# Performance work log

Measured on AMD Instinct MI355X. Metric: run time of the kernel, lower is better.

The kernel has to match this reference:

```python
import jax, jax.numpy as jnp
import numpy as np
from jax import lax

TAU_MIN = 0.01
TAU_MAX = 10.0
SLOW_TAU = 5.0


def setup_inputs() -> dict:
    key = jax.random.key(0)
    ks = iter(jax.random.split(key, 40))
    def p(shape, scale=0.05):
        return (jax.random.normal(next(ks), shape, jnp.float32) * scale)
    B, T, D = 1024, 512, 31
    FU, SU, H = 32, 32, 64
    inp = {
        "x": jax.random.normal(next(ks), (B, T, D), jnp.float32),
        # FlashFloodGate: Linear(62->32), Linear(32->1)
        "fg_w1": p((32, 2 * D)), "fg_b1": p((32,)),
        "fg_w2": p((1, 32)), "fg_b2": p((1,)),
        # fast LTC cell
        "fwin": p((FU, D)), "fbin": p((FU,)), "fwrec": p((FU, FU)),
        # slow LTC cell
        "swin": p((SU, D)), "sbin": p((SU,)), "swrec": p((SU, SU)),
        # fusion Linear(64->64)
        "fu_w": p((H, FU + SU)), "fu_b": p((H,)),
        # attention Linear(64->32), Linear(32->1)
        "at_w1": p((32, H)), "at_b1": p((32,)),
        "at_w2": p((1, 32)), "at_b2": p((1,)),
        # depth head Linear(64->64), Linear(64->5)
        "d_w1": p((64, H)), "d_b1": p((64,)),
        "d_w2": p((5, 64)), "d_b2": p((5,)),
        # overflow head Linear(64->64), Linear(64->32), Linear(32->1)
        "o_w1": p((64, H)), "o_b1": p((64,)),
        "o_w2": p((32, 64)), "o_b2": p((32,)),
        "o_w3": p((1, 32)), "o_b3": p((1,)),
        # intensity head Linear(64->32), Linear(32->1)
        "i_w1": p((32, H)), "i_b1": p((32,)),
        "i_w2": p((1, 32)), "i_b2": p((1,)),
    }
    return inp


def _ltc_scan(pre_tbh, w_rec, tau_tb1, h0):
    # pre_tbh: [T,B,H] precomputed W_in x + b; tau_tb1 broadcastable to [T,B,1]
    def step(h, inp):
        pre_t, tau_t = inp
        upd = jnp.tanh(pre_t + h @ w_rec.T)
        h = h + (upd - h) / tau_t
        return h, h
    _, hs = lax.scan(step, h0, (pre_tbh, tau_tb1))
    return jnp.transpose(hs, (1, 0, 2))  # [B,T,H]


def _forward(x, fg_w1, fg_b1, fg_w2, fg_b2, fwin, fbin, fwrec, swin, sbin, swrec,
             fu_w, fu_b, at_w1, at_b1, at_w2, at_b2, d_w1, d_b1, d_w2, d_b2,
             o_w1, o_b1, o_w2, o_b2, o_w3, o_b3, i_w1, i_b1, i_w2, i_b2):
    B, T, D = x.shape
    # FlashFloodGate over all timesteps (x_prev of t=0 is x_0 -> dx=0)
    dx = jnp.concatenate([jnp.zeros_like(x[:, :1]), x[:, 1:] - x[:, :-1]], axis=1)
    ci = jnp.concatenate([x, dx], axis=-1)                       # [B,T,2D]
    cs = jax.nn.sigmoid(jnp.tanh(ci @ fg_w1.T + fg_b1) @ fg_w2.T + fg_b2)  # [B,T,1]
    tau_fast = TAU_MAX - cs * (TAU_MAX - TAU_MIN)                # [B,T,1]
    # fast LTC (stepwise tau)
    pre_f = jnp.transpose(x @ fwin.T + fbin, (1, 0, 2))          # [T,B,FU]
    fast = _ltc_scan(pre_f, fwrec, jnp.transpose(tau_fast, (1, 0, 2)),
                     jnp.zeros((B, fwrec.shape[0]), x.dtype))
    # slow LTC (constant tau = 5.0, shape [B,1])
    pre_s = jnp.transpose(x @ swin.T + sbin, (1, 0, 2))          # [T,B,SU]
    slow = _ltc_scan(pre_s, swrec, jnp.full((T, 1, 1), SLOW_TAU, x.dtype),
                     jnp.zeros((B, swrec.shape[0]), x.dtype))
    # fusion
    ltc = jnp.tanh(jnp.concatenate([fast, slow], axis=-1) @ fu_w.T + fu_b)  # [B,T,H]
    # attention over time
    logits = jnp.tanh(ltc @ at_w1.T + at_b1) @ at_w2.T + at_b2   # [B,T,1]
    attn = jax.nn.softmax(logits, axis=1)
    context = jnp.sum(ltc * attn, axis=1)                        # [B,H]
    # heads (dropout is identity in eval)
    depths = jax.nn.relu(context @ d_w1.T + d_b1) @ d_w2.T + d_b2
    overflow = jax.nn.sigmoid(
        jax.nn.relu(jax.nn.relu(context @ o_w1.T + o_b1) @ o_w2.T + o_b2) @ o_w3.T + o_b3)
    intensity = jax.nn.sigmoid(jax.nn.relu(context @ i_w1.T + i_b1) @ i_w2.T + i_b2)
    return (depths, overflow, intensity)


def reference(x, fg_w1, fg_b1, fg_w2, fg_b2, fwin, fbin, fwrec, swin, sbin, swrec,
              fu_w, fu_b, at_w1, at_b1, at_w2, at_b2, d_w1, d_b1, d_w2, d_b2,
              o_w1, o_b1, o_w2, o_b2, o_w3, o_b3, i_w1, i_b1, i_w2, i_b2):
    return _forward(x, fg_w1, fg_b1, fg_w2, fg_b2, fwin, fbin, fwrec, swin, sbin,
                    swrec, fu_w, fu_b, at_w1, at_b1, at_w2, at_b2, d_w1, d_b1,
                    d_w2, d_b2, o_w1, o_b1, o_w2, o_b2, o_w3, o_b3,
                    i_w1, i_b1, i_w2, i_b2)
```

## Files before the change

kernel.cpp:

```cpp
#include <hip/hip_runtime.h>


#define T_  512
#define D_  31
#define GR_ 16
#define NG_ 32
#define NIT 35
#define L2E 1.4426950408889634f
#define TS_ 2.8853900817779268f

typedef decltype(__builtin_amdgcn_cvt_pkrtz(0.0f, 0.0f)) h2;
typedef _Float16 h8v __attribute__((ext_vector_type(8)));
typedef float    f4v __attribute__((ext_vector_type(4)));

__device__ __forceinline__ float fexp2(float x){ return __builtin_amdgcn_exp2f(x); }
__device__ __forceinline__ float frcp (float x){ return __builtin_amdgcn_rcpf(x); }
__device__ __forceinline__ float tanh_pre(float x){
    return 1.0f - 2.0f * frcp(1.0f + fexp2(x));
}
__device__ __forceinline__ h2 cvt2(float a, float b){ return __builtin_amdgcn_cvt_pkrtz(a, b); }
__device__ __forceinline__ h2 bch2(unsigned v){ return __builtin_bit_cast(h2, v); }
__device__ __forceinline__ unsigned bcu(h2 v){ return __builtin_bit_cast(unsigned, v); }

template <int CTRL>
__device__ __forceinline__ float dppf(float v){
    int r = __builtin_amdgcn_update_dpp(0, __builtin_bit_cast(int, v),
                                        CTRL, 0xf, 0xf, true);
    return __builtin_bit_cast(float, r);
}
template <int CTRL>
__device__ __forceinline__ unsigned dppu(unsigned v){
    return (unsigned)__builtin_amdgcn_update_dpp(0, (int)v, CTRL, 0xf, 0xf, true);
}
__device__ __forceinline__ unsigned swz16(unsigned v){
    return (unsigned)__builtin_amdgcn_ds_swizzle((int)v, 0x401F);
}
__device__ __forceinline__ float rsum16(float v){
    v += dppf<0xB1>(v); v += dppf<0x4E>(v); v += dppf<0x141>(v); v += dppf<0x140>(v);
    return v;
}

#if __has_builtin(__builtin_amdgcn_fdot2)
#define FDOT2(acc, a, b) (acc) = __builtin_amdgcn_fdot2((a), (b), (acc), false)
#else
#define FDOT2(acc, a, b) (acc) += (float)(a)[0]*(float)(b)[0] + (float)(a)[1]*(float)(b)[1]
#endif

#define MFMA16(A, Bf, Cf) __builtin_amdgcn_mfma_f32_16x16x32_f16((A), (Bf), (Cf), 0, 0, 0)

#define BAR() do { asm volatile("s_waitcnt lgkmcnt(0)" ::: "memory"); \
                   __builtin_amdgcn_s_barrier();                      \
                   asm volatile("" ::: "memory"); } while (0)

__launch_bounds__(256, 4)
__global__ void lnn_mf(
    const float* __restrict__ X,
    const float* __restrict__ fg_w1, const float* __restrict__ fg_b1,
    const float* __restrict__ fg_w2, const float* __restrict__ fg_b2,
    const float* __restrict__ fwin,  const float* __restrict__ fbin,
    const float* __restrict__ fwrec,
    const float* __restrict__ swin,  const float* __restrict__ sbin,
    const float* __restrict__ swrec,
    const float* __restrict__ fu_w,  const float* __restrict__ fu_b,
    const float* __restrict__ at_w1, const float* __restrict__ at_b1,
    const float* __restrict__ at_w2, const float* __restrict__ at_b2,
    const float* __restrict__ d_w1,  const float* __restrict__ d_b1,
    const float* __restrict__ d_w2,  const float* __restrict__ d_b2,
    const float* __restrict__ o_w1,  const float* __restrict__ o_b1,
    const float* __restrict__ o_w2,  const float* __restrict__ o_b2,
    const float* __restrict__ o_w3,  const float* __restrict__ o_b3,
    const float* __restrict__ i_w1,  const float* __restrict__ i_b1,
    const float* __restrict__ i_w2,  const float* __restrict__ i_b2,
    float* __restrict__ out, int B)
{
    const int b    = blockIdx.x;
    const int tx   = threadIdx.x;
    const int wid  = tx >> 6;
    const int lane = tx & 63;
    const int u    = lane & 31;
    const int hb32 = lane & 32;
    const int role = (wid + b) & 3;

    __shared__ __align__(16) float    xr_sh [4][GR_][36];
    __shared__ float    xdm   [36];
    __shared__ __align__(16) float    pre_t [2][64][20];
    __shared__ __align__(16) float    rt4   [2][GR_];
    __shared__ __align__(16) unsigned hpk_sh[2][GR_][36];
    __shared__ __align__(16) unsigned ltcpk [2][GR_][36];
    __shared__ __align__(16) float    pw_sh [GR_];
    __shared__ float    ctx_sh[64];

    if (tx < 64) xr_sh[tx >> 4][tx & 15][31] = 0.0f;

    if (role == 0) {
        const int col = lane & 15, kb = lane >> 4;
        h8v wB[8];
        #pragma unroll
        for (int c = 0; c < 8; ++c) {
            float wv[8];
            #pragma unroll
            for (int j = 0; j < 8; ++j) {
                const int k = kb*8 + j;
                float v = 0.0f;
                if (k < 31) {
                    const int uu = 16*(c & 1) + col;
                    if (c < 2)      v = fg_w1[uu*62 + k] + fg_w1[uu*62 + 31 + k];
                    else if (c < 4) v = fg_w1[uu*62 + 31 + k];
                    else if (c < 6) v = fwin[uu*31 + k];
                    else            v = swin[uu*31 + k];
                }
                wv[j] = v * TS_;
            }
            uint4 qq = { bcu(cvt2(wv[0],wv[1])), bcu(cvt2(wv[2],wv[3])),
                         bcu(cvt2(wv[4],wv[5])), bcu(cvt2(wv[6],wv[7])) };
            wB[c] = __builtin_bit_cast(h8v, qq);
        }
        const float b1c[2] = { fg_b1[col] * TS_, fg_b1[16 + col] * TS_ };
        const float pb[4]  = { fbin[col] * TS_, fbin[16+col] * TS_,
                               sbin[col] * TS_, sbin[16+col] * TS_ };
        const float w2n[2] = { fg_w2[col] * (-L2E), fg_w2[16+col] * (-L2E) };
        const float b2n    = fg_b2[0] * (-L2E);
        const unsigned* Xu = (const unsigned*)(X + (size_t)b * T_ * D_ + lane);
        float ypv[2] = {0.0f, 0.0f};
        asm volatile("s_waitcnt vmcnt(0)" ::: "memory");

        #pragma unroll
        for (int gg = 0; gg < 2; ++gg)
            #pragma unroll
            for (int k = 0; k < GR_; ++k)
                if (lane < 31)
                    __builtin_amdgcn_global_load_lds(
                        (const __attribute__((address_space(1))) unsigned*)(Xu + (size_t)(GR_*gg + k) * 31),
                        (__attribute__((address_space(3))) unsigned*)(&xr_sh[gg][k][0]),
                        4, 0, 0);

        for (int i = 0; i < NIT; ++i) {
            asm volatile("s_waitcnt vmcnt(16)" ::: "memory");
            BAR();
            {
                const int gq = i + 2;
                #pragma unroll
                for (int k = 0; k < GR_; ++k) {
                    int tl = GR_*gq + k; if (tl > 511) tl = 511;
                    float* dst = (gq <= NG_-1) ? &xr_sh[gq & 3][k][0] : &xdm[0];
                    if (lane < 31)
                        __builtin_amdgcn_global_load_lds(
                            (const __attribute__((address_space(1))) unsigned*)(Xu + (size_t)tl * 31),
                            (__attribute__((address_space(3))) unsigned*)dst,
                            4, 0, 0);
                }
            }
            if (i <= NG_-1) {
                const int sG = i & 3;
                const int sP = i & 1;
                const float* xrow = &xr_sh[sG][col][kb*8];
                float4 xa = *(const float4*)xrow;
                float4 xb = *(const float4*)(xrow + 4);
                uint4 aq = { bcu(cvt2(xa.x,xa.y)), bcu(cvt2(xa.z,xa.w)),
                             bcu(cvt2(xb.x,xb.y)), bcu(cvt2(xb.z,xb.w)) };
                h8v Af = __builtin_bit_cast(h8v, aq);
                f4v C[8];
                #pragma unroll
                for (int c = 0; c < 8; ++c) {
                    f4v z = {0.f, 0.f, 0.f, 0.f};
                    C[c] = MFMA16(Af, wB[c], z);
                }
                const int tb = kb * 4;
                float tp[4] = {0.f, 0.f, 0.f, 0.f};
                #pragma unroll
                for (int p = 0; p < 2; ++p) {
                    f4v G = C[p], Y = C[2+p];
                    if (i == 0) ypv[p] = __shfl(Y[0], col);
                    float ylast = __shfl(Y[3], 48 + col);
                    float yup   = __shfl(Y[3], (lane - 16) & 63);
                    float ysh0  = (kb == 0) ? ypv[p] : yup;
                    float h1v[4];
                    h1v[0] = tanh_pre(G[0] - ysh0 + b1c[p]);
                    h1v[1] = tanh_pre(G[1] - Y[0] + b1c[p]);
                    h1v[2] = tanh_pre(G[2] - Y[1] + b1c[p]);
                    h1v[3] = tanh_pre(G[3] - Y[2] + b1c[p]);
                    ypv[p] = ylast;
                    #pragma unroll
                    for (int r = 0; r < 4; ++r) tp[r] += h1v[r] * w2n[p];
                }
                float4 rtq;
                #pragma unroll
                for (int r = 0; r < 4; ++r) {
                    float s  = rsum16(tp[r]) + b2n;
                    float cs = frcp(1.0f + fexp2(s));
                    float rt = frcp(10.0f - 9.99f * cs);
                    ((float*)&rtq)[r] = rt;
                }
                if (col == 0) *(float4*)&rt4[sP][tb] = rtq;
                #pragma unroll
                for (int c = 4; c < 8; ++c) {
                    const int uo = (c < 6 ? 0 : 32) + 16*(c & 1) + col;
                    #pragma unroll
                    for (int r = 0; r < 4; ++r)
                        pre_t[sP][uo][tb + r] = C[c][r] + pb[c-4];
                }
            }
        }
        asm volatile("s_waitcnt vmcnt(0)" ::: "memory");
    } else if (role == 1) {
        const bool slow = (lane >= 32);
        const float* W  = (slow ? swrec : fwrec) + u * 32;
        const int M0[8] = {0,2,7,5,15,13,8,10};
        const int M1[8] = {1,3,6,4,14,12,9,11};
        h2 wr[16];
        #pragma unroll
        for (int j = 0; j < 16; ++j) {
            const int x = (j & 8) ? 16 : 0;
            wr[j] = cvt2(W[u ^ M0[j & 7] ^ x] * TS_, W[u ^ M1[j & 7] ^ x] * TS_);
        }
        float h_st = 0.0f;

        for (int i = 0; i < NIT; ++i) {
            BAR();
            if (i >= 1 && i <= NG_) {
                const int gR = i - 1;
                const int sP = gR & 1;
                const int sH = gR & 1;
                const float4* pp = (const float4*)(&pre_t[sP][lane][0]);
                float4 p0 = pp[0], p1 = pp[1], p2 = pp[2], p3 = pp[3];
                const float4* rr = (const float4*)(&rt4[sP][0]);
                float4 r0 = rr[0], r1 = rr[1], r2 = rr[2], r3 = rr[3];
                float preA[GR_] = { p0.x,p0.y,p0.z,p0.w, p1.x,p1.y,p1.z,p1.w,
                                    p2.x,p2.y,p2.z,p2.w, p3.x,p3.y,p3.z,p3.w };
                float rtA[GR_]  = { r0.x,r0.y,r0.z,r0.w, r1.x,r1.y,r1.z,r1.w,
                                    r2.x,r2.y,r2.z,r2.w, r3.x,r3.y,r3.z,r3.w };
                #pragma unroll
                for (int k = 0; k < GR_; ++k) if (slow) rtA[k] = 0.2f;
                __builtin_amdgcn_s_setprio(1);
                #pragma unroll
                for (int k = 0; k < GR_; ++k) {
                    float hn = dppf<0xB1>(h_st);
                    unsigned u0 = bcu(cvt2(h_st, hn));
                    unsigned w0 = swz16(u0);
                    unsigned u1 = dppu<0x4E>(u0);
                    unsigned u2 = dppu<0x141>(u0);
                    unsigned u3 = dppu<0x141>(u1);
                    unsigned u4 = dppu<0x140>(u0);
                    unsigned u5 = dppu<0x140>(u1);
                    unsigned u6 = dppu<0x140>(u2);
                    unsigned u7 = dppu<0x140>(u3);
                    unsigned w1 = dppu<0x4E>(w0);
                    unsigned w2 = dppu<0x141>(w0);
                    unsigned w3 = dppu<0x141>(w1);
                    unsigned w4 = dppu<0x140>(w0);
                    unsigned w5 = dppu<0x140>(w1);
                    unsigned w6 = dppu<0x140>(w2);
                    unsigned w7 = dppu<0x140>(w3);
                    float a0 = 0.f, a1 = 0.f, a2 = 0.f, a3 = 0.f;
                    FDOT2(a0, bch2(u0), wr[0]);  FDOT2(a1, bch2(u1), wr[1]);
                    FDOT2(a2, bch2(u2), wr[2]);  FDOT2(a3, bch2(u3), wr[3]);
                    FDOT2(a0, bch2(u4), wr[4]);  FDOT2(a1, bch2(u5), wr[5]);
                    FDOT2(a2, bch2(u6), wr[6]);  FDOT2(a3, bch2(u7), wr[7]);
                    FDOT2(a0, bch2(w0), wr[8]);  FDOT2(a1, bch2(w1), wr[9]);
                    FDOT2(a2, bch2(w2), wr[10]); FDOT2(a3, bch2(w3), wr[11]);
                    FDOT2(a0, bch2(w4), wr[12]); FDOT2(a1, bch2(w5), wr[13]);
                    FDOT2(a2, bch2(w6), wr[14]); FDOT2(a3, bch2(w7), wr[15]);
                    float v   = (a0 + a1) + (a2 + a3);
                    float upd = tanh_pre(v + preA[k]);
                    h_st += (upd - h_st) * rtA[k];
                    float hw = dppf<0xB1>(h_st);
                    if (!(lane & 1))
                        hpk_sh[sH][k][lane >> 1] = bcu(cvt2(h_st, hw));
                }
                __builtin_amdgcn_s_setprio(0);
            }
        }
    } else if (role == 2) {
        const int col = lane & 15, kb = lane >> 4;
        h8v wF[8];
        #pragma unroll
        for (int kc = 0; kc < 2; ++kc)
            #pragma unroll
            for (int nc = 0; nc < 4; ++nc) {
                float wv[8];
                #pragma unroll
                for (int j = 0; j < 8; ++j)
                    wv[j] = fu_w[(16*nc + col)*64 + 32*kc + 8*kb + j] * TS_;
                uint4 qq = { bcu(cvt2(wv[0],wv[1])), bcu(cvt2(wv[2],wv[3])),
                             bcu(cvt2(wv[4],wv[5])), bcu(cvt2(wv[6],wv[7])) };
                wF[kc*4 + nc] = __builtin_bit_cast(h8v, qq);
            }
        const float fb4[4] = { fu_b[col] * TS_, fu_b[16+col] * TS_,
                               fu_b[32+col] * TS_, fu_b[48+col] * TS_ };

        for (int i = 0; i < NIT; ++i) {
            BAR();
            if (i >= 2 && i <= NG_ + 1) {
                const int gF = i - 2;
                const int sH = gF & 1;
                const unsigned* hrow = &hpk_sh[sH][col][0];
                uint4 a0q = *(const uint4*)(hrow + kb*4);
                uint4 a1q = *(const uint4*)(hrow + kb*4 + 16);
                h8v A0 = __builtin_bit_cast(h8v, a0q);
                h8v A1 = __builtin_bit_cast(h8v, a1q);
                const int tb = kb * 4;
                #pragma unroll
                for (int nc = 0; nc < 4; ++nc) {
                    f4v c4 = {0.f, 0.f, 0.f, 0.f};
                    c4 = MFMA16(A0, wF[nc],     c4);
                    c4 = MFMA16(A1, wF[4 + nc], c4);
                    #pragma unroll
                    for (int r = 0; r < 4; ++r) {
                        float v  = tanh_pre(c4[r] + fb4[nc]);
                        float vn = dppf<0xB1>(v);
                        h2 pk = (col & 1) ? cvt2(vn, v) : cvt2(v, vn);
                        if (!(col & 1))
                            ltcpk[gF & 1][tb + r][(16*nc + col) >> 1] = bcu(pk);
                    }
                }
            }
        }
    } else {
        const int col = lane & 15, kb = lane >> 4;
        h8v wA[4];
        #pragma unroll
        for (int kt = 0; kt < 2; ++kt)
            #pragma unroll
            for (int nt = 0; nt < 2; ++nt) {
                float wv[8];
                #pragma unroll
                for (int j = 0; j < 8; ++j)
                    wv[j] = at_w1[(nt*16 + col)*64 + kt*32 + 8*kb + j] * TS_;
                uint4 qq = { bcu(cvt2(wv[0],wv[1])), bcu(cvt2(wv[2],wv[3])),
                             bcu(cvt2(wv[4],wv[5])), bcu(cvt2(wv[6],wv[7])) };
                wA[kt*2 + nt] = __builtin_bit_cast(h8v, qq);
            }
        const float ab1v[2] = { at_b1[col] * TS_, at_b1[16 + col] * TS_ };
        const float w2L[2]  = { at_w2[col] * L2E, at_w2[16 + col] * L2E };
        const float ab2L    = at_b2[0] * L2E;
        float s_run = 0.0f, c_run = 0.0f;

        for (int i = 0; i < NIT; ++i) {
            BAR();
            if (i >= 3) {
                const int gA = i - 3;
                const int sl = gA & 1;
                const unsigned* lrow = &ltcpk[sl][col][0];
                uint4 l0q = *(const uint4*)(lrow + kb*4);
                uint4 l1q = *(const uint4*)(lrow + kb*4 + 16);
                h8v L0 = __builtin_bit_cast(h8v, l0q);
                h8v L1 = __builtin_bit_cast(h8v, l1q);
                f4v CA[2];
                #pragma unroll
                for (int nt = 0; nt < 2; ++nt) {
                    f4v c4 = {0.f, 0.f, 0.f, 0.f};
                    c4 = MFMA16(L0, wA[nt],     c4);
                    c4 = MFMA16(L1, wA[2 + nt], c4);
                    CA[nt] = c4;
                }
                float4 pwq;
                #pragma unroll
                for (int r = 0; r < 4; ++r) {
                    float s = tanh_pre(CA[0][r] + ab1v[0]) * w2L[0]
                            + tanh_pre(CA[1][r] + ab1v[1]) * w2L[1];
                    s = rsum16(s);
                    ((float*)&pwq)[r] = fexp2(s + ab2L);
                }
                if (col == 0) *(float4*)&pw_sh[kb*4] = pwq;
                const float4* pwp = (const float4*)&pw_sh[0];
                float4 q0 = pwp[0], q1 = pwp[1], q2 = pwp[2], q3 = pwp[3];
                float pwA[GR_] = { q0.x,q0.y,q0.z,q0.w, q1.x,q1.y,q1.z,q1.w,
                                   q2.x,q2.y,q2.z,q2.w, q3.x,q3.y,q3.z,q3.w };
                #pragma unroll
                for (int t = 0; t < GR_; ++t) {
                    float ltc = (float)((const _Float16*)(&ltcpk[sl][t][0]))[lane];
                    s_run += pwA[t];
                    c_run += pwA[t] * ltc;
                }
            }
        }
        ctx_sh[lane] = c_run * frcp(s_run);
    }

    __syncthreads();

    if (wid == 0) {
        float r1 = d_b1[lane];
        #pragma unroll
        for (int c = 0; c < 16; ++c) {
            float4 cq = ((const float4*)ctx_sh)[c];
            float4 wq = ((const float4*)(d_w1 + lane*64))[c];
            r1 += wq.x*cq.x + wq.y*cq.y + wq.z*cq.z + wq.w*cq.w;
        }
        r1 = fmaxf(r1, 0.0f);
        #pragma unroll
        for (int kk = 0; kk < 5; ++kk) {
            float v = d_w2[kk*64 + lane] * r1;
            v += __shfl_xor(v, 1);  v += __shfl_xor(v, 2);
            v += __shfl_xor(v, 4);  v += __shfl_xor(v, 8);
            v += __shfl_xor(v, 16); v += __shfl_xor(v, 32);
            if (lane == 0) out[b*5 + kk] = v + d_b2[kk];
        }
    } else if (wid == 1) {
        float r1 = o_b1[lane];
        #pragma unroll
        for (int c = 0; c < 16; ++c) {
            float4 cq = ((const float4*)ctx_sh)[c];
            float4 wq = ((const float4*)(o_w1 + lane*64))[c];
            r1 += wq.x*cq.x + wq.y*cq.y + wq.z*cq.z + wq.w*cq.w;
        }
        r1 = fmaxf(r1, 0.0f);
        float acc = 0.0f;
        #pragma unroll
        for (int j = 0; j < 32; ++j) {
            float rj = __shfl(r1, hb32 + j);
            acc += o_w2[u*64 + hb32 + j] * rj;
        }
        acc += __shfl_xor(acc, 32);
        float r2 = fmaxf(acc + o_b2[u], 0.0f);
        float v  = o_w3[u] * r2;
        v += __shfl_xor(v, 1);  v += __shfl_xor(v, 2);
        v += __shfl_xor(v, 4);  v += __shfl_xor(v, 8);
        v += __shfl_xor(v, 16);
        if (lane == 0) {
            float e = fexp2((v + o_b3[0]) * -L2E);
            out[5*B + b] = frcp(1.0f + e);
        }
    } else if (wid == 2) {
        float acc = 0.0f;
        #pragma unroll
        for (int c = 0; c < 8; ++c) {
            float4 cq = ((const float4*)(ctx_sh + hb32))[c];
            float4 wq = ((const float4*)(i_w1 + u*64 + hb32))[c];
            acc += wq.x*cq.x + wq.y*cq.y + wq.z*cq.z + wq.w*cq.w;
        }
        acc += __shfl_xor(acc, 32);
        float r1 = fmaxf(acc + i_b1[u], 0.0f);
        float v  = i_w2[u] * r1;
        v += __shfl_xor(v, 1);  v += __shfl_xor(v, 2);
        v += __shfl_xor(v, 4);  v += __shfl_xor(v, 8);
        v += __shfl_xor(v, 16);
        if (lane == 0) {
            float e = fexp2((v + i_b2[0]) * -L2E);
            out[6*B + b] = frcp(1.0f + e);
        }
    }
}

extern "C" void kernel_launch(void* const* d_in, const int* in_sizes, int n_in,
                              void* d_out, int out_size, void* d_ws, size_t ws_size,
                              hipStream_t stream) {
    (void)n_in; (void)out_size; (void)d_ws; (void)ws_size;
    const float* X     = (const float*)d_in[0];
    const float* fg_w1 = (const float*)d_in[1];
    const float* fg_b1 = (const float*)d_in[2];
    const float* fg_w2 = (const float*)d_in[3];
    const float* fg_b2 = (const float*)d_in[4];
    const float* fwin  = (const float*)d_in[5];
    const float* fbin  = (const float*)d_in[6];
    const float* fwrec = (const float*)d_in[7];
    const float* swin  = (const float*)d_in[8];
    const float* sbin  = (const float*)d_in[9];
    const float* swrec = (const float*)d_in[10];
    const float* fu_w  = (const float*)d_in[11];
    const float* fu_b  = (const float*)d_in[12];
    const float* at_w1 = (const float*)d_in[13];
    const float* at_b1 = (const float*)d_in[14];
    const float* at_w2 = (const float*)d_in[15];
    const float* at_b2 = (const float*)d_in[16];
    const float* d_w1  = (const float*)d_in[17];
    const float* d_b1  = (const float*)d_in[18];
    const float* d_w2  = (const float*)d_in[19];
    const float* d_b2  = (const float*)d_in[20];
    const float* o_w1  = (const float*)d_in[21];
    const float* o_b1  = (const float*)d_in[22];
    const float* o_w2  = (const float*)d_in[23];
    const float* o_b2  = (const float*)d_in[24];
    const float* o_w3  = (const float*)d_in[25];
    const float* o_b3  = (const float*)d_in[26];
    const float* i_w1  = (const float*)d_in[27];
    const float* i_b1  = (const float*)d_in[28];
    const float* i_w2  = (const float*)d_in[29];
    const float* i_b2  = (const float*)d_in[30];
    float* out = (float*)d_out;

    const int B = in_sizes[0] / (T_ * D_);
    dim3 grid(B), block(256);
    hipLaunchKernelGGL(lnn_mf, grid, block, 0, stream,
        X, fg_w1, fg_b1, fg_w2, fg_b2, fwin, fbin, fwrec, swin, sbin, swrec,
        fu_w, fu_b, at_w1, at_b1, at_w2, at_b2, d_w1, d_b1, d_w2, d_b2,
        o_w1, o_b1, o_w2, o_b2, o_w3, o_b3, i_w1, i_b1, i_w2, i_b2, out, B);
}
```

Measured before the change: 99.71 us.

## Deepen producer-to-recurrence pipeline with 4-slot pre buffer and transposed layout

The input-projection stage now writes its results into a 4-deep ring buffer laid out [slot][t][unit] with padding, and the recurrence stage consumes them two iterations later instead of one. Downstream fusion and attention stages shift by one iteration, and the loop count grows by one. The intent is to take the projection/tau computation off the critical path of the serial recurrence wave and to change the LDS access pattern to per-timestep rows. In exchange the recurrence wave does 16 scalar LDS reads instead of 4 vector reads, and there is one extra barrier iteration.

```diff
diff --git a/kernel.cpp b/kernel.cpp
--- a/kernel.cpp
+++ b/kernel.cpp
@@ -5,7 +5,7 @@
 #define D_  31
 #define GR_ 16
 #define NG_ 32
-#define NIT 35
+#define NIT 36
 #define L2E 1.4426950408889634f
 #define TS_ 2.8853900817779268f
 
@@ -83,8 +83,8 @@
 
     __shared__ __align__(16) float    xr_sh [4][GR_][36];
     __shared__ float    xdm   [36];
-    __shared__ __align__(16) float    pre_t [2][64][20];
-    __shared__ __align__(16) float    rt4   [2][GR_];
+    __shared__ float    pre_sh[4][GR_][65];
+    __shared__ __align__(16) float    rt_sh [4][GR_];
     __shared__ __align__(16) unsigned hpk_sh[2][GR_][36];
     __shared__ __align__(16) unsigned ltcpk [2][GR_][36];
     __shared__ __align__(16) float    pw_sh [GR_];
@@ -152,7 +152,6 @@
             }
             if (i <= NG_-1) {
                 const int sG = i & 3;
-                const int sP = i & 1;
                 const float* xrow = &xr_sh[sG][col][kb*8];
                 float4 xa = *(const float4*)xrow;
                 float4 xb = *(const float4*)(xrow + 4);
@@ -188,16 +187,15 @@
                 for (int r = 0; r < 4; ++r) {
                     float s  = rsum16(tp[r]) + b2n;
                     float cs = frcp(1.0f + fexp2(s));
-                    float rt = frcp(10.0f - 9.99f * cs);
-                    ((float*)&rtq)[r] = rt;
-                }
-                if (col == 0) *(float4*)&rt4[sP][tb] = rtq;
+                    ((float*)&rtq)[r] = frcp(10.0f - 9.99f * cs);
+                }
+                if (col == 0) *(float4*)&rt_sh[sG][tb] = rtq;
                 #pragma unroll
                 for (int c = 4; c < 8; ++c) {
                     const int uo = (c < 6 ? 0 : 32) + 16*(c & 1) + col;
                     #pragma unroll
                     for (int r = 0; r < 4; ++r)
-                        pre_t[sP][uo][tb + r] = C[c][r] + pb[c-4];
+                        pre_sh[sG][tb + r][uo] = C[c][r] + pb[c-4];
                 }
             }
         }
@@ -217,20 +215,23 @@
 
         for (int i = 0; i < NIT; ++i) {
             BAR();
-            if (i >= 1 && i <= NG_) {
-                const int gR = i - 1;
-                const int sP = gR & 1;
+            if (i >= 2 && i <= NG_ + 1) {
+                const int gR = i - 2;
+                const int sR = gR & 3;
                 const int sH = gR & 1;
-                const float4* pp = (const float4*)(&pre_t[sP][lane][0]);
-                float4 p0 = pp[0], p1 = pp[1], p2 = pp[2], p3 = pp[3];
-                const float4* rr = (const float4*)(&rt4[sP][0]);
+                float preA[GR_], rtA[GR_];
+                #pragma unroll
+                for (int k = 0; k < GR_; ++k)
+                    preA[k] = pre_sh[sR][k][lane];
+                const float4* rr = (const float4*)(&rt_sh[sR][0]);
                 float4 r0 = rr[0], r1 = rr[1], r2 = rr[2], r3 = rr[3];
-                float preA[GR_] = { p0.x,p0.y,p0.z,p0.w, p1.x,p1.y,p1.z,p1.w,
-                                    p2.x,p2.y,p2.z,p2.w, p3.x,p3.y,p3.z,p3.w };
-                float rtA[GR_]  = { r0.x,r0.y,r0.z,r0.w, r1.x,r1.y,r1.z,r1.w,
-                                    r2.x,r2.y,r2.z,r2.w, r3.x,r3.y,r3.z,r3.w };
-                #pragma unroll
-                for (int k = 0; k < GR_; ++k) if (slow) rtA[k] = 0.2f;
+                {
+                    float tmp[GR_] = { r0.x,r0.y,r0.z,r0.w, r1.x,r1.y,r1.z,r1.w,
+                                       r2.x,r2.y,r2.z,r2.w, r3.x,r3.y,r3.z,r3.w };
+                    #pragma unroll
+                    for (int k = 0; k < GR_; ++k)
+                        rtA[k] = slow ? 0.2f : tmp[k];
+                }
                 __builtin_amdgcn_s_setprio(1);
                 #pragma unroll
                 for (int k = 0; k < GR_; ++k) {
@@ -290,8 +291,8 @@
 
         for (int i = 0; i < NIT; ++i) {
             BAR();
-            if (i >= 2 && i <= NG_ + 1) {
-                const int gF = i - 2;
+            if (i >= 3 && i <= NG_ + 2) {
+                const int gF = i - 3;
                 const int sH = gF & 1;
                 const unsigned* hrow = &hpk_sh[sH][col][0];
                 uint4 a0q = *(const uint4*)(hrow + kb*4);
@@ -337,8 +338,8 @@
 
         for (int i = 0; i < NIT; ++i) {
             BAR();
-            if (i >= 3) {
-                const int gA = i - 3;
+            if (i >= 4) {
+                const int gA = i - 4;
                 const int sl = gA & 1;
                 const unsigned* lrow = &ltcpk[sl][col][0];
                 uint4 l0q = *(const uint4*)(lrow + kb*4);
```

Measured after the change: 94.41 us, median of 2. 1.06x faster.
